# Performance work log

Measured on AMD Instinct MI355X. Metric: run time of the kernel, lower is better.

The kernel has to match this reference:

```python
import jax, jax.numpy as jnp
import numpy as np

N, P, T, D = 25000, 100000, 4, 128
DIN = 4 * D + 4  # 516
LEAKY = 0.001


def setup_inputs() -> dict:
    key = jax.random.key(0)
    ks = jax.random.split(key, 12)
    inp = {
        "coords": jax.random.normal(ks[0], (N, T, 3), jnp.float32),
        "propers": jax.random.randint(ks[1], (P, 4), 0, N, jnp.int64),
        "encoded": jax.random.normal(ks[2], (N, D), jnp.float32),
        "t": jax.random.uniform(ks[3], (T,), jnp.float32),
        "answer": jax.random.normal(ks[4], (N, T, 3), jnp.float32),
        # AggregateMLP(516 -> 128 -> 128 -> 128 -> 2), LeakyReLU(0.001) between
        "W0": jax.random.normal(ks[5], (DIN, D), jnp.float32) / np.sqrt(DIN),
        "b0": jnp.zeros((D,), jnp.float32),
        "W1": jax.random.normal(ks[6], (D, D), jnp.float32) / np.sqrt(D),
        "b1": jnp.zeros((D,), jnp.float32),
        "W2": jax.random.normal(ks[7], (D, D), jnp.float32) / np.sqrt(D),
        "b2": jnp.zeros((D,), jnp.float32),
        "W3": jax.random.normal(ks[8], (D, 2), jnp.float32) / np.sqrt(D),
        "b3": jnp.zeros((2,), jnp.float32),
    }
    return inp


def _forward(coords, propers, encoded, t, answer, W0, b0, W1, b1, W2, b2, W3, b3):
    p0, p1, p2, p3 = propers[:, 0], propers[:, 1], propers[:, 2], propers[:, 3]
    c0, c1, c2, c3 = coords[p0], coords[p1], coords[p2], coords[p3]  # [P,T,3]
    u1 = c1 - c0
    u2 = c2 - c1
    u3 = c3 - c2
    u1xu2 = jnp.cross(u1, u2, axis=-1)
    u2xu3 = jnp.cross(u2, u3, axis=-1)
    u2_norm = jnp.linalg.norm(u2, axis=-1, keepdims=True)
    u1yu2 = u1 * u2_norm
    theta = jnp.arctan2((u1yu2 * u2xu3).sum(-1), (u1xu2 * u2xu3).sum(-1))  # [P,T]
    dr = c0 - c3  # [P,T,3]
    dl = jnp.sqrt(jnp.clip(jnp.square(dr).sum(-1), 1e-12))  # [P,T]
    dh = dr / dl[..., None]

    Pn, Tn = propers.shape[0], t.shape[0]
    bcast = lambda e: jnp.broadcast_to(e[:, None, :], (Pn, Tn, e.shape[-1]))
    feats = jnp.concatenate(
        [
            bcast(encoded[p0]),
            bcast(encoded[p1]),
            bcast(encoded[p2]),
            bcast(encoded[p3]),
            jnp.broadcast_to(t.reshape(1, Tn, 1), (Pn, Tn, 1)),
            jnp.sin(theta)[..., None],
            jnp.cos(theta)[..., None],
            dl[..., None],
        ],
        axis=2,
    )  # [P,T,516]

    h = jax.nn.leaky_relu(feats @ W0 + b0, LEAKY)
    h = jax.nn.leaky_relu(h @ W1 + b1, LEAKY)
    h = jax.nn.leaky_relu(h @ W2 + b2, LEAKY)
    delta = h @ W3 + b3  # [P,T,2]

    out = answer.at[p0].add(-0.5 * delta[:, :, 0:1] * dh)
    out = out.at[p3].add(0.5 * delta[:, :, 1:2] * dh)
    return out


def reference(coords, propers, encoded, t, answer, W0, b0, W1, b1, W2, b2, W3, b3):
    return _forward(coords, propers, encoded, t, answer, W0, b0, W1, b1, W2, b2, W3, b3)
```

## Files before the change

kernel.cpp:

```cpp
#include <hip/hip_runtime.h>
#include <hip/hip_bf16.h>

#define NN 25000
#define PP 100000
#define TT 4
#define DD 128
#define LEAKY 0.001f

#define PB 16
#define ROWS 64

typedef __bf16 bf16;
typedef __bf16 bf16x8 __attribute__((ext_vector_type(8)));
typedef float  f32x4  __attribute__((ext_vector_type(4)));

#define OFF_ENCB  0u
#define OFF_W0SW  6400000u
#define OFF_W1SW  6531072u
#define OFF_W2SW  6563840u
#define OFF_W3SW  6596608u
#define WS_END    6600704u

#define PR_ENCB4 800000
#define PR_W0SW  65536
#define PR_W1SW  16384
#define PR_W2SW  16384
#define PR_W3SW  2048
#define PR_COPY4 75000
#define PR_TOTAL (PR_ENCB4 + PR_W0SW + PR_W1SW + PR_W2SW + PR_W3SW + PR_COPY4)

__global__ __launch_bounds__(256) void prep_kernel(
    const float* __restrict__ encoded, const float* __restrict__ W0,
    const float* __restrict__ W1, const float* __restrict__ W2,
    const float* __restrict__ W3, const float* __restrict__ answer,
    bf16* __restrict__ encB, bf16* __restrict__ W0sw, bf16* __restrict__ W1sw,
    bf16* __restrict__ W2sw, bf16* __restrict__ W3sw, float* __restrict__ out)
{
    int idx = blockIdx.x * 256 + threadIdx.x;
    if (idx < PR_ENCB4) {
        float4 v = ((const float4*)encoded)[idx];
        bf16 pk[4] = {(bf16)v.x, (bf16)v.y, (bf16)v.z, (bf16)v.w};
        *(uint2*)(encB + idx * 4) = *(const uint2*)pk;
        return;
    }
    idx -= PR_ENCB4;
    if (idx < PR_W0SW) {
        int j = idx & 7, lane = (idx >> 3) & 63, c = idx >> 9;
        int fr = lane & 15, quad = lane >> 4;
        int kc = c & 15, iwv = c >> 4;
        int k = kc * 32 + quad * 8 + j;
        W0sw[idx] = (bf16)W0[k * 128 + iwv * 16 + fr];
        return;
    }
    idx -= PR_W0SW;
    if (idx < PR_W1SW) {
        int j = idx & 7, lane = (idx >> 3) & 63, c = idx >> 9;
        int fr = lane & 15, quad = lane >> 4;
        int kc = c & 3, nt = c >> 2;
        int k = kc * 32 + quad * 8 + j;
        W1sw[idx] = (bf16)W1[k * 128 + nt * 16 + fr];
        return;
    }
    idx -= PR_W1SW;
    if (idx < PR_W2SW) {
        int j = idx & 7, lane = (idx >> 3) & 63, c = idx >> 9;
        int fr = lane & 15, quad = lane >> 4;
        int kc = c & 3, nt = c >> 2;
        int k = kc * 32 + quad * 8 + j;
        W2sw[idx] = (bf16)W2[k * 128 + nt * 16 + fr];
        return;
    }
    idx -= PR_W2SW;
    if (idx < PR_W3SW) {
        int j = idx & 7, lane = (idx >> 3) & 63, kc = idx >> 9;
        int fr = lane & 15, quad = lane >> 4;
        int k = kc * 32 + quad * 8 + j;
        W3sw[idx] = (fr < 2) ? (bf16)W3[k * 2 + fr] : (bf16)0.0f;
        return;
    }
    idx -= PR_W3SW;
    if (idx < PR_COPY4) { ((float4*)out)[idx] = ((const float4*)answer)[idx]; }
}

__global__ __launch_bounds__(512, 8) void main_kernel(
    const float* __restrict__ coords, const int* __restrict__ propers,
    const float* __restrict__ tvec, const float* __restrict__ W0,
    const float* __restrict__ b0, const float* __restrict__ b1,
    const float* __restrict__ b2, const float* __restrict__ b3,
    const bf16* __restrict__ encB, const bf16* __restrict__ W0sw,
    const bf16* __restrict__ W1sw, const bf16* __restrict__ W2sw,
    const bf16* __restrict__ W3sw, float* __restrict__ out)
{
    __shared__ bf16 sAH[8704];
    #define SA(p, c) sAH[(p) * 520 + (c)]
    #define SH(r, j) sAH[(r) * 136 + (j)]
    __shared__ int   sNodes[PB][4];
    __shared__ float sSn[ROWS], sCs[ROWS], sDl[ROWS], sDh[ROWS][3];
    __shared__ float sDelta[ROWS][2];

    const int tid  = threadIdx.x;
    const int pBase = blockIdx.x * PB;
    const float tv0 = tvec[0], tv1 = tvec[1], tv2 = tvec[2], tv3 = tvec[3];

    {
        int row = tid >> 3, sg = tid & 7;
        int p = row >> 2, i = row & 3;
        int node = propers[(pBase + p) * 4 + i];
        if (sg == 0) sNodes[p][i] = node;
        const uint4* src = (const uint4*)(encB + (size_t)node * 128 + sg * 16);
        uint4* dst = (uint4*)(&SA(p, i * 128 + sg * 16));
        dst[0] = src[0];
        dst[1] = src[1];
    }
    if (tid < ROWS) {
        int r = tid, p = r >> 2, t = r & 3;
        const int* prow = propers + (pBase + p) * 4;
        int n0 = prow[0], n1 = prow[1], n2 = prow[2], n3 = prow[3];
        const float* c0 = coords + n0 * 12 + t * 3;
        const float* c1 = coords + n1 * 12 + t * 3;
        const float* c2 = coords + n2 * 12 + t * 3;
        const float* c3 = coords + n3 * 12 + t * 3;
        float u1x = c1[0]-c0[0], u1y = c1[1]-c0[1], u1z = c1[2]-c0[2];
        float u2x = c2[0]-c1[0], u2y = c2[1]-c1[1], u2z = c2[2]-c1[2];
        float u3x = c3[0]-c2[0], u3y = c3[1]-c2[1], u3z = c3[2]-c2[2];
        float ax = u1y*u2z - u1z*u2y, ay = u1z*u2x - u1x*u2z, az = u1x*u2y - u1y*u2x;
        float bx = u2y*u3z - u2z*u3y, by = u2z*u3x - u2x*u3z, bz = u2x*u3y - u2y*u3x;
        float u2n = sqrtf(u2x*u2x + u2y*u2y + u2z*u2z);
        float num = u2n * (u1x*bx + u1y*by + u1z*bz);
        float den = ax*bx + ay*by + az*bz;
        float hyp = sqrtf(num*num + den*den);
        float sn, cs;
        if (hyp > 1e-30f) { float ih = 1.0f / hyp; sn = num * ih; cs = den * ih; }
        else { sn = 0.0f; cs = 1.0f; }
        float drx = c0[0]-c3[0], dry = c0[1]-c3[1], drz = c0[2]-c3[2];
        float dl = sqrtf(fmaxf(drx*drx + dry*dry + drz*drz, 1e-12f));
        float il = 1.0f / dl;
        sSn[r] = sn; sCs[r] = cs; sDl[r] = dl;
        sDh[r][0] = drx * il; sDh[r][1] = dry * il; sDh[r][2] = drz * il;
    }
    __syncthreads();

    const int wv = tid >> 6, lane = tid & 63;
    const int fr = lane & 15;
    const int quad = lane >> 4;
    const int m4 = wv & 3;
    const int nh = wv >> 2;

    f32x4 acc = {0.f,0.f,0.f,0.f};
    {
        const bf16* aBase = &SA(fr, quad * 8);
        const bf16* w0b = W0sw + (size_t)wv * 16 * 512 + lane * 8;
        #pragma unroll
        for (int kc = 0; kc < 16; ++kc) {
            bf16x8 aF = *(const bf16x8*)(aBase + kc * 32);
            bf16x8 bF = *(const bf16x8*)(w0b + kc * 512);
            acc = __builtin_amdgcn_mfma_f32_16x16x32_bf16(aF, bF, acc, 0, 0, 0);
        }
    }
    __syncthreads();

    {
        int j = wv * 16 + fr;
        float w512 = W0[512 * 128 + j], w513 = W0[513 * 128 + j];
        float w514 = W0[514 * 128 + j], w515 = W0[515 * 128 + j];
        float bb = b0[j];
        #pragma unroll
        for (int reg = 0; reg < 4; ++reg) {
            int p = quad * 4 + reg;
            float g = acc[reg];
            #pragma unroll
            for (int t = 0; t < 4; ++t) {
                int r = p * 4 + t;
                float tvv = (t == 0) ? tv0 : (t == 1) ? tv1 : (t == 2) ? tv2 : tv3;
                float v = g + tvv * w512 + sSn[r] * w513 + sCs[r] * w514 + sDl[r] * w515 + bb;
                v = v > 0.0f ? v : LEAKY * v;
                SH(r, j) = (bf16)v;
            }
        }
    }
    __syncthreads();

    f32x4 hacc[4];
    #pragma unroll
    for (int nt = 0; nt < 4; ++nt) hacc[nt] = (f32x4){0.f,0.f,0.f,0.f};
    {
        const bf16* aRow = &SH(m4 * 16 + fr, quad * 8);
        const bf16* w1b = W1sw + lane * 8;
        #pragma unroll
        for (int kc = 0; kc < 4; ++kc) {
            bf16x8 aF = *(const bf16x8*)(aRow + kc * 32);
            #pragma unroll
            for (int nt = 0; nt < 4; ++nt) {
                bf16x8 bF = *(const bf16x8*)(w1b + ((nh * 4 + nt) * 4 + kc) * 512);
                hacc[nt] = __builtin_amdgcn_mfma_f32_16x16x32_bf16(aF, bF, hacc[nt], 0, 0, 0);
            }
        }
    }
    __syncthreads();
    #pragma unroll
    for (int nt = 0; nt < 4; ++nt) {
        int j = (nh * 4 + nt) * 16 + fr;
        float bb = b1[j];
        #pragma unroll
        for (int reg = 0; reg < 4; ++reg) {
            int r = m4 * 16 + quad * 4 + reg;
            float v = hacc[nt][reg] + bb;
            v = v > 0.0f ? v : LEAKY * v;
            SH(r, j) = (bf16)v;
        }
    }
    __syncthreads();

    #pragma unroll
    for (int nt = 0; nt < 4; ++nt) hacc[nt] = (f32x4){0.f,0.f,0.f,0.f};
    {
        const bf16* aRow = &SH(m4 * 16 + fr, quad * 8);
        const bf16* w2b = W2sw + lane * 8;
        #pragma unroll
        for (int kc = 0; kc < 4; ++kc) {
            bf16x8 aF = *(const bf16x8*)(aRow + kc * 32);
            #pragma unroll
            for (int nt = 0; nt < 4; ++nt) {
                bf16x8 bF = *(const bf16x8*)(w2b + ((nh * 4 + nt) * 4 + kc) * 512);
                hacc[nt] = __builtin_amdgcn_mfma_f32_16x16x32_bf16(aF, bF, hacc[nt], 0, 0, 0);
            }
        }
    }
    __syncthreads();
    #pragma unroll
    for (int nt = 0; nt < 4; ++nt) {
        int j = (nh * 4 + nt) * 16 + fr;
        float bb = b2[j];
        #pragma unroll
        for (int reg = 0; reg < 4; ++reg) {
            int r = m4 * 16 + quad * 4 + reg;
            float v = hacc[nt][reg] + bb;
            v = v > 0.0f ? v : LEAKY * v;
            SH(r, j) = (bf16)v;
        }
    }
    __syncthreads();

    if (wv < 4) {
        f32x4 dacc = {0.f,0.f,0.f,0.f};
        const bf16* aRow = &SH(wv * 16 + fr, quad * 8);
        const bf16* w3b = W3sw + lane * 8;
        #pragma unroll
        for (int kc = 0; kc < 4; ++kc) {
            bf16x8 aF = *(const bf16x8*)(aRow + kc * 32);
            bf16x8 bF = *(const bf16x8*)(w3b + kc * 512);
            dacc = __builtin_amdgcn_mfma_f32_16x16x32_bf16(aF, bF, dacc, 0, 0, 0);
        }
        if (fr < 2) {
            float bb = b3[fr];
            #pragma unroll
            for (int reg = 0; reg < 4; ++reg)
                sDelta[wv * 16 + quad * 4 + reg][fr] = dacc[reg] + bb;
        }
    }
    __syncthreads();

    if (tid < ROWS * 6) {
        int r = tid / 6, c = tid % 6;
        int p = r >> 2, t = r & 3;
        int side = c / 3, ax = c % 3;
        int node = sNodes[p][side ? 3 : 0];
        float dval = side ? 0.5f * sDelta[r][1] : -0.5f * sDelta[r][0];
        atomicAdd(out + node * 12 + t * 3 + ax, dval * sDh[r][ax]);
    }
    #undef SA
    #undef SH
}

extern "C" void kernel_launch(void* const* d_in, const int* in_sizes, int n_in,
                              void* d_out, int out_size, void* d_ws, size_t ws_size,
                              hipStream_t stream) {
    const float* coords  = (const float*)d_in[0];
    const int*   propers = (const int*)d_in[1];
    const float* encoded = (const float*)d_in[2];
    const float* tvec    = (const float*)d_in[3];
    const float* answer  = (const float*)d_in[4];
    const float* W0 = (const float*)d_in[5];
    const float* b0 = (const float*)d_in[6];
    const float* W1 = (const float*)d_in[7];
    const float* b1 = (const float*)d_in[8];
    const float* W2 = (const float*)d_in[9];
    const float* b2 = (const float*)d_in[10];
    const float* W3 = (const float*)d_in[11];
    const float* b3 = (const float*)d_in[12];
    float* out = (float*)d_out;
    char* ws = (char*)d_ws;
    bf16* encB = (bf16*)(ws + OFF_ENCB);
    bf16* W0sw = (bf16*)(ws + OFF_W0SW);
    bf16* W1sw = (bf16*)(ws + OFF_W1SW);
    bf16* W2sw = (bf16*)(ws + OFF_W2SW);
    bf16* W3sw = (bf16*)(ws + OFF_W3SW);

    int prep_blocks = (PR_TOTAL + 255) / 256;
    prep_kernel<<<prep_blocks, 256, 0, stream>>>(encoded, W0, W1, W2, W3, answer,
                                                 encB, W0sw, W1sw, W2sw, W3sw, out);
    main_kernel<<<PP / PB, 512, 0, stream>>>(coords, propers, tvec, W0, b0, b1, b2, b3,
                                             encB, W0sw, W1sw, W2sw, W3sw, out);
}
```

Before: 197.6 us.

## Double per-block propers to 32 and ping-pong shared buffers to drop barriers

Each block now processes 32 propers (128 rows) instead of 16. Every W0 fragment loaded from global feeds two MFMAs, and W1/W2 fragments are reused across two row tiles per wave, which raises weight reuse per block. Two shared buffers alternate between layers so each layer's epilogue writes straight into the other buffer, removing several __syncthreads. In exchange the block uses more LDS, launch bounds drop to 4 blocks per CU, and half as many blocks are launched, which lowers occupancy and the number of blocks available to hide gather latency.

```diff
diff --git a/kernel.cpp b/kernel.cpp
--- a/kernel.cpp
+++ b/kernel.cpp
@@ -7,8 +7,8 @@
 #define DD 128
 #define LEAKY 0.001f
 
-#define PB 16
-#define ROWS 64
+#define PB 32
+#define ROWS 128
 
 typedef __bf16 bf16;
 typedef __bf16 bf16x8 __attribute__((ext_vector_type(8)));
@@ -82,7 +82,7 @@
     if (idx < PR_COPY4) { ((float4*)out)[idx] = ((const float4*)answer)[idx]; }
 }
 
-__global__ __launch_bounds__(512, 8) void main_kernel(
+__global__ __launch_bounds__(512, 4) void main_kernel(
     const float* __restrict__ coords, const int* __restrict__ propers,
     const float* __restrict__ tvec, const float* __restrict__ W0,
     const float* __restrict__ b0, const float* __restrict__ b1,
@@ -91,9 +91,11 @@
     const bf16* __restrict__ W1sw, const bf16* __restrict__ W2sw,
     const bf16* __restrict__ W3sw, float* __restrict__ out)
 {
-    __shared__ bf16 sAH[8704];
-    #define SA(p, c) sAH[(p) * 520 + (c)]
-    #define SH(r, j) sAH[(r) * 136 + (j)]
+    __shared__ bf16 sBuf0[ROWS * 136];
+    __shared__ bf16 sBuf1[ROWS * 136];
+    #define SA(p, c)  sBuf1[(p) * 520 + (c)]
+    #define SH0(r, j) sBuf0[(r) * 136 + (j)]
+    #define SH1(r, j) sBuf1[(r) * 136 + (j)]
     __shared__ int   sNodes[PB][4];
     __shared__ float sSn[ROWS], sCs[ROWS], sDl[ROWS], sDh[ROWS][3];
     __shared__ float sDelta[ROWS][2];
@@ -103,14 +105,14 @@
     const float tv0 = tvec[0], tv1 = tvec[1], tv2 = tvec[2], tv3 = tvec[3];
 
     {
-        int row = tid >> 3, sg = tid & 7;
+        int row = tid >> 2, sg = tid & 3;
         int p = row >> 2, i = row & 3;
         int node = propers[(pBase + p) * 4 + i];
         if (sg == 0) sNodes[p][i] = node;
-        const uint4* src = (const uint4*)(encB + (size_t)node * 128 + sg * 16);
-        uint4* dst = (uint4*)(&SA(p, i * 128 + sg * 16));
-        dst[0] = src[0];
-        dst[1] = src[1];
+        const uint4* src = (const uint4*)(encB + (size_t)node * 128 + sg * 32);
+        uint4* dst = (uint4*)(&SA(p, i * 128 + sg * 32));
+        #pragma unroll
+        for (int q = 0; q < 4; ++q) dst[q] = src[q];
     }
     if (tid < ROWS) {
         int r = tid, p = r >> 2, t = r & 3;
@@ -143,48 +145,55 @@
     const int wv = tid >> 6, lane = tid & 63;
     const int fr = lane & 15;
     const int quad = lane >> 4;
-    const int m4 = wv & 3;
-    const int nh = wv >> 2;
-
-    f32x4 acc = {0.f,0.f,0.f,0.f};
+
+    f32x4 acc0 = {0.f,0.f,0.f,0.f}, acc1 = {0.f,0.f,0.f,0.f};
     {
-        const bf16* aBase = &SA(fr, quad * 8);
+        const bf16* aB0 = &SA(fr, quad * 8);
+        const bf16* aB1 = &SA(16 + fr, quad * 8);
         const bf16* w0b = W0sw + (size_t)wv * 16 * 512 + lane * 8;
         #pragma unroll
         for (int kc = 0; kc < 16; ++kc) {
-            bf16x8 aF = *(const bf16x8*)(aBase + kc * 32);
-            bf16x8 bF = *(const bf16x8*)(w0b + kc * 512);
-            acc = __builtin_amdgcn_mfma_f32_16x16x32_bf16(aF, bF, acc, 0, 0, 0);
-        }
-    }
-    __syncthreads();
-
+            bf16x8 bF  = *(const bf16x8*)(w0b + kc * 512);
+            bf16x8 aF0 = *(const bf16x8*)(aB0 + kc * 32);
+            bf16x8 aF1 = *(const bf16x8*)(aB1 + kc * 32);
+            acc0 = __builtin_amdgcn_mfma_f32_16x16x32_bf16(aF0, bF, acc0, 0, 0, 0);
+            acc1 = __builtin_amdgcn_mfma_f32_16x16x32_bf16(aF1, bF, acc1, 0, 0, 0);
+        }
+    }
     {
         int j = wv * 16 + fr;
         float w512 = W0[512 * 128 + j], w513 = W0[513 * 128 + j];
         float w514 = W0[514 * 128 + j], w515 = W0[515 * 128 + j];
         float bb = b0[j];
         #pragma unroll
-        for (int reg = 0; reg < 4; ++reg) {
-            int p = quad * 4 + reg;
-            float g = acc[reg];
-            #pragma unroll
-            for (int t = 0; t < 4; ++t) {
-                int r = p * 4 + t;
-                float tvv = (t == 0) ? tv0 : (t == 1) ? tv1 : (t == 2) ? tv2 : tv3;
-                float v = g + tvv * w512 + sSn[r] * w513 + sCs[r] * w514 + sDl[r] * w515 + bb;
-                v = v > 0.0f ? v : LEAKY * v;
-                SH(r, j) = (bf16)v;
-            }
-        }
-    }
-    __syncthreads();
-
-    f32x4 hacc[4];
+        for (int s = 0; s < 2; ++s) {
+            const f32x4 a = s ? acc1 : acc0;
+            #pragma unroll
+            for (int reg = 0; reg < 4; ++reg) {
+                int p = s * 16 + quad * 4 + reg;
+                float g = a[reg] + bb;
+                #pragma unroll
+                for (int t = 0; t < 4; ++t) {
+                    int r = p * 4 + t;
+                    float tvv = (t == 0) ? tv0 : (t == 1) ? tv1 : (t == 2) ? tv2 : tv3;
+                    float v = g + tvv * w512 + sSn[r] * w513 + sCs[r] * w514 + sDl[r] * w515;
+                    v = fmaxf(v, LEAKY * v);
+                    SH0(r, j) = (bf16)v;
+                }
+            }
+        }
+    }
+    __syncthreads();
+
+    const int m2 = (wv & 3) * 2;
+    const int nh = wv >> 2;
+
     #pragma unroll
-    for (int nt = 0; nt < 4; ++nt) hacc[nt] = (f32x4){0.f,0.f,0.f,0.f};
-    {
-        const bf16* aRow = &SH(m4 * 16 + fr, quad * 8);
+    for (int s = 0; s < 2; ++s) {
+        f32x4 hacc[4];
+        #pragma unroll
+        for (int nt = 0; nt < 4; ++nt) hacc[nt] = (f32x4){0.f,0.f,0.f,0.f};
+        const bf16* aRow = &SH0((m2 + s) * 16 + fr, quad * 8);
         const bf16* w1b = W1sw + lane * 8;
         #pragma unroll
         for (int kc = 0; kc < 4; ++kc) {
@@ -195,26 +204,27 @@
                 hacc[nt] = __builtin_amdgcn_mfma_f32_16x16x32_bf16(aF, bF, hacc[nt], 0, 0, 0);
             }
         }
-    }
-    __syncthreads();
+        #pragma unroll
+        for (int nt = 0; nt < 4; ++nt) {
+            int j = (nh * 4 + nt) * 16 + fr;
+            float bb = b1[j];
+            #pragma unroll
+            for (int reg = 0; reg < 4; ++reg) {
+                int r = (m2 + s) * 16 + quad * 4 + reg;
+                float v = hacc[nt][reg] + bb;
+                v = fmaxf(v, LEAKY * v);
+                SH1(r, j) = (bf16)v;
+            }
+        }
+    }
+    __syncthreads();
+
     #pragma unroll
-    for (int nt = 0; nt < 4; ++nt) {
-        int j = (nh * 4 + nt) * 16 + fr;
-        float bb = b1[j];
-        #pragma unroll
-        for (int reg = 0; reg < 4; ++reg) {
-            int r = m4 * 16 + quad * 4 + reg;
-            float v = hacc[nt][reg] + bb;
-            v = v > 0.0f ? v : LEAKY * v;
-            SH(r, j) = (bf16)v;
-        }
-    }
-    __syncthreads();
-
-    #pragma unroll
-    for (int nt = 0; nt < 4; ++nt) hacc[nt] = (f32x4){0.f,0.f,0.f,0.f};
-    {
-        const bf16* aRow = &SH(m4 * 16 + fr, quad * 8);
+    for (int s = 0; s < 2; ++s) {
+        f32x4 hacc[4];
+        #pragma unroll
+        for (int nt = 0; nt < 4; ++nt) hacc[nt] = (f32x4){0.f,0.f,0.f,0.f};
+        const bf16* aRow = &SH1((m2 + s) * 16 + fr, quad * 8);
         const bf16* w2b = W2sw + lane * 8;
         #pragma unroll
         for (int kc = 0; kc < 4; ++kc) {
@@ -225,25 +235,24 @@
                 hacc[nt] = __builtin_amdgcn_mfma_f32_16x16x32_bf16(aF, bF, hacc[nt], 0, 0, 0);
             }
         }
-    }
-    __syncthreads();
-    #pragma unroll
-    for (int nt = 0; nt < 4; ++nt) {
-        int j = (nh * 4 + nt) * 16 + fr;
-        float bb = b2[j];
-        #pragma unroll
-        for (int reg = 0; reg < 4; ++reg) {
-            int r = m4 * 16 + quad * 4 + reg;
-            float v = hacc[nt][reg] + bb;
-            v = v > 0.0f ? v : LEAKY * v;
-            SH(r, j) = (bf16)v;
-        }
-    }
-    __syncthreads();
-
-    if (wv < 4) {
+        #pragma unroll
+        for (int nt = 0; nt < 4; ++nt) {
+            int j = (nh * 4 + nt) * 16 + fr;
+            float bb = b2[j];
+            #pragma unroll
+            for (int reg = 0; reg < 4; ++reg) {
+                int r = (m2 + s) * 16 + quad * 4 + reg;
+                float v = hacc[nt][reg] + bb;
+                v = fmaxf(v, LEAKY * v);
+                SH0(r, j) = (bf16)v;
+            }
+        }
+    }
+    __syncthreads();
+
+    {
         f32x4 dacc = {0.f,0.f,0.f,0.f};
-        const bf16* aRow = &SH(wv * 16 + fr, quad * 8);
+        const bf16* aRow = &SH0(wv * 16 + fr, quad * 8);
         const bf16* w3b = W3sw + lane * 8;
         #pragma unroll
         for (int kc = 0; kc < 4; ++kc) {
@@ -260,8 +269,8 @@
     }
     __syncthreads();
 
-    if (tid < ROWS * 6) {
-        int r = tid / 6, c = tid % 6;
+    for (int idx = tid; idx < ROWS * 6; idx += 512) {
+        int r = idx / 6, c = idx % 6;
         int p = r >> 2, t = r & 3;
         int side = c / 3, ax = c % 3;
         int node = sNodes[p][side ? 3 : 0];
@@ -269,7 +278,8 @@
         atomicAdd(out + node * 12 + t * 3 + ax, dval * sDh[r][ax]);
     }
     #undef SA
-    #undef SH
+    #undef SH0
+    #undef SH1
 }
 
 extern "C" void kernel_launch(void* const* d_in, const int* in_sizes, int n_in,
```

Measured after the change: 206.2 us. +4.3%, slower.
